# Kernel optimization log

Hardware: AMD Instinct MI355X
Metric: run time of the kernel (lower is better)

The kernel has to match this reference:

```python
import jax, jax.numpy as jnp
import numpy as np

N_NODES = 100000
HIDDEN = 64
IN_CH = 128
N_EDGES = 1600000


def setup_inputs() -> dict:
    key = jax.random.key(0)
    ks = jax.random.split(key, 12)
    x = jax.random.normal(ks[0], (N_NODES, IN_CH), dtype=jnp.float32)
    edge_index = jax.random.randint(ks[1], (2, N_EDGES), 0, N_NODES, dtype=jnp.int64)

    def glorot(k, fan_in, fan_out):
        s = jnp.sqrt(6.0 / (fan_in + fan_out)).astype(jnp.float32)
        return jax.random.uniform(k, (fan_in, fan_out), jnp.float32, -s, s)

    return {
        "x": x,
        "edge_index": edge_index,
        # GCNConv layer 1: linear (no bias) + post-aggregation bias
        "W1": glorot(ks[2], IN_CH, HIDDEN),
        "b1": jnp.zeros((HIDDEN,), jnp.float32),
        # GCNConv layer 2
        "W2": glorot(ks[3], HIDDEN, HIDDEN),
        "b2": jnp.zeros((HIDDEN,), jnp.float32),
        # edge classifier MLP: Linear(2H,H) -> ReLU -> Linear(H,2)
        "Wc1": glorot(ks[4], 2 * HIDDEN, HIDDEN),
        "bc1": jnp.zeros((HIDDEN,), jnp.float32),
        "Wc2": glorot(ks[5], HIDDEN, 2),
        "bc2": jnp.zeros((2,), jnp.float32),
    }


def _gcn_forward(x, edge_index, W1, b1, W2, b2, Wc1, bc1, Wc2, bc2):
    n = x.shape[0]
    src, dst = edge_index[0], edge_index[1]
    # add self-loops (PyG GCNConv default)
    loop = jnp.arange(n, dtype=edge_index.dtype)
    a_src = jnp.concatenate([src, loop])  # [E+N]
    a_dst = jnp.concatenate([dst, loop])
    # symmetric normalization: deg over destination with unit edge weights
    deg = jax.ops.segment_sum(jnp.ones(a_dst.shape[0], x.dtype), a_dst, num_segments=n)
    dis = jax.lax.rsqrt(deg)  # deg >= 1 due to self-loops
    norm = dis[a_src] * dis[a_dst]  # [E+N]

    def conv(h, W, b):
        h = h @ W  # [N, H]
        msg = h[a_src] * norm[:, None]  # [E+N, H] gather + scale
        return jax.ops.segment_sum(msg, a_dst, num_segments=n) + b

    h = jax.nn.relu(conv(x, W1, b1))  # dropout is identity in eval mode
    h = conv(h, W2, b2)
    # edge classifier on concatenated endpoint embeddings
    e = jnp.concatenate([h[src], h[dst]], axis=1)  # [E, 2H]
    z = jax.nn.relu(e @ Wc1 + bc1)
    return z @ Wc2 + bc2  # [E, 2]


def reference(x, edge_index, W1, b1, W2, b2, Wc1, bc1, Wc2, bc2):
    return _gcn_forward(x, edge_index, W1, b1, W2, b2, Wc1, bc1, Wc2, bc2)
```

## Files before the change

### kernel.cpp

```cpp
#include <hip/hip_runtime.h>
#include <hip/hip_fp16.h>

#define HID 64
#define BKT_SHIFT 10
#define BKT_NODES 1024
#define PCHUNKS 512

typedef _Float16 half8 __attribute__((ext_vector_type(8)));
typedef _Float16 half4 __attribute__((ext_vector_type(4)));
typedef float f32x4 __attribute__((ext_vector_type(4)));
typedef float f32x2 __attribute__((ext_vector_type(2)));

__global__ __launch_bounds__(256) void k_bkt_count(const int* __restrict__ dst,
                                                   int* __restrict__ G, int E,
                                                   int nbkt, int chunk) {
  __shared__ int hist[128];
  int p = blockIdx.x, tid = threadIdx.x;
  for (int i = tid; i < nbkt; i += 256) hist[i] = 0;
  __syncthreads();
  int s = p * chunk, e = min(s + chunk, E);
  for (int i = s + tid; i < e; i += 256) atomicAdd(&hist[dst[i] >> BKT_SHIFT], 1);
  __syncthreads();
  for (int b = tid; b < nbkt; b += 256) G[b * PCHUNKS + p] = hist[b];
}

__global__ void k_scan1(const int* __restrict__ in, int* __restrict__ scanout,
                        int* __restrict__ blocksums, int n) {
  __shared__ int sdata[256];
  int tid = threadIdx.x;
  int base = blockIdx.x * 1024 + tid * 4;
  int v0 = 0, v1 = 0, v2 = 0, v3 = 0;
  if (base + 0 < n) v0 = in[base + 0];
  if (base + 1 < n) v1 = in[base + 1];
  if (base + 2 < n) v2 = in[base + 2];
  if (base + 3 < n) v3 = in[base + 3];
  int tsum = v0 + v1 + v2 + v3;
  sdata[tid] = tsum;
  __syncthreads();
  for (int off = 1; off < 256; off <<= 1) {
    int t = (tid >= off) ? sdata[tid - off] : 0;
    __syncthreads();
    sdata[tid] += t;
    __syncthreads();
  }
  int excl = sdata[tid] - tsum;
  if (base + 0 < n) scanout[base + 0] = excl;
  if (base + 1 < n) scanout[base + 1] = excl + v0;
  if (base + 2 < n) scanout[base + 2] = excl + v0 + v1;
  if (base + 3 < n) scanout[base + 3] = excl + v0 + v1 + v2;
  if (tid == 255) blocksums[blockIdx.x] = sdata[255];
}

__global__ void k_scan2(int* blocksums, int nb) {
  __shared__ int s[128];
  int tid = threadIdx.x;
  int v = (tid < nb) ? blocksums[tid] : 0;
  s[tid] = v;
  __syncthreads();
  for (int off = 1; off < 128; off <<= 1) {
    int t = (tid >= off) ? s[tid - off] : 0;
    __syncthreads();
    s[tid] += t;
    __syncthreads();
  }
  if (tid < nb) blocksums[tid] = s[tid] - v;
}

__global__ void k_scan3(const int* __restrict__ scanout,
                        const int* __restrict__ blocksums, int* __restrict__ outp,
                        int n) {
  int i = blockIdx.x * blockDim.x + threadIdx.x;
  if (i < n) outp[i] = scanout[i] + blocksums[i >> 10];
}

__global__ __launch_bounds__(256) void k_bkt_scatter(
    const int* __restrict__ src, const int* __restrict__ dst,
    const int* __restrict__ Gscan, int* __restrict__ psrc,
    unsigned short* __restrict__ pdst, int E, int nbkt, int chunk) {
  __shared__ int gbase[128];
  __shared__ int rcnt[128];
  int p = blockIdx.x, tid = threadIdx.x;
  for (int b = tid; b < nbkt; b += 256) {
    gbase[b] = Gscan[b * PCHUNKS + p];
    rcnt[b] = 0;
  }
  __syncthreads();
  int s = p * chunk, e = min(s + chunk, E);
  for (int i = s + tid; i < e; i += 256) {
    int d = dst[i];
    int b = d >> BKT_SHIFT;
    int r = atomicAdd(&rcnt[b], 1);
    int pos = gbase[b] + r;
    psrc[pos] = src[i];
    pdst[pos] = (unsigned short)(d & (BKT_NODES - 1));
  }
}

__global__ __launch_bounds__(1024) void k_bkt_final(
    const int* __restrict__ Gscan, const int* __restrict__ psrc,
    const unsigned short* __restrict__ pdst, int* __restrict__ rowoff,
    float* __restrict__ dis, int* __restrict__ csr_src, int E, int nbkt, int N) {
  __shared__ int cnt[BKT_NODES];
  __shared__ int lo[BKT_NODES];
  int b = blockIdx.x, tid = threadIdx.x;
  int s = Gscan[b * PCHUNKS];
  int eend = (b + 1 < nbkt) ? Gscan[(b + 1) * PCHUNKS] : E;
  cnt[tid] = 0;
  __syncthreads();
  for (int i = s + tid; i < eend; i += 1024) atomicAdd(&cnt[pdst[i]], 1);
  __syncthreads();
  int v = cnt[tid];
  lo[tid] = v;
  __syncthreads();
  for (int off = 1; off < 1024; off <<= 1) {
    int t = (tid >= off) ? lo[tid - off] : 0;
    __syncthreads();
    lo[tid] += t;
    __syncthreads();
  }
  int excl = lo[tid] - v;
  int node = b * BKT_NODES + tid;
  if (node < N) {
    rowoff[node] = s + excl;
    dis[node] = rsqrtf((float)v + 1.0f);
  }
  __syncthreads();
  lo[tid] = excl;
  cnt[tid] = 0;
  __syncthreads();
  for (int i = s + tid; i < eend; i += 1024) {
    int ln = pdst[i];
    int r = atomicAdd(&cnt[ln], 1);
    csr_src[s + lo[ln] + r] = psrc[i];
  }
}

__global__ void k_pack_all(const float* __restrict__ W1, const float* __restrict__ W2,
                           const float* __restrict__ Wc1, const float* __restrict__ bc1,
                           __half* __restrict__ packW1, __half* __restrict__ packW2,
                           __half* __restrict__ packUV, float* __restrict__ biasUV,
                           __half* __restrict__ ysent) {
  int b = blockIdx.x, tid = threadIdx.x;
  if (b < 4) {
    int t = b * 256 + tid;
    int f = t >> 6, L = t & 63;
    int kc = f >> 2, nb = f & 3;
    int k = 32 * kc + ((L >> 4) << 3);
    int n = (L & 15) + 16 * nb;
    for (int j = 0; j < 8; ++j)
      packW1[(t << 3) + j] = __float2half(W1[(k + j) * 64 + n]);
  } else if (b < 6) {
    int t = (b - 4) * 256 + tid;
    int f = t >> 6, L = t & 63;
    int kc = f >> 2, nb = f & 3;
    int k = 32 * kc + ((L >> 4) << 3);
    int n = (L & 15) + 16 * nb;
    for (int j = 0; j < 8; ++j)
      packW2[(t << 3) + j] = __float2half(W2[(k + j) * 64 + n]);
  } else if (b < 10) {
    int t = (b - 6) * 256 + tid;
    int f = t >> 6, L = t & 63;
    int kc = f >> 3, nb = f & 7;
    int k = 32 * kc + ((L >> 4) << 3);
    int n = (L & 15) + 16 * nb;
    for (int j = 0; j < 8; ++j) {
      float w = (n < 64) ? Wc1[(k + j) * 64 + n] : Wc1[(64 + k + j) * 64 + (n - 64)];
      packUV[(t << 3) + j] = __float2half(w);
    }
  } else {
    if (tid < 128) biasUV[tid] = (tid < 64) ? bc1[tid] : 0.f;
    else if (tid < 192) ysent[tid - 128] = __float2half(0.f);
  }
}

template <int K, int NOUT, bool F32IN>
__global__ __launch_bounds__(256) void k_lin_mfma(
    const void* __restrict__ Xv, const __half* __restrict__ packB,
    const float* __restrict__ bias, const float* __restrict__ dis,
    __half* __restrict__ Y, int n) {
  int wid = blockIdx.x * 4 + (threadIdx.x >> 6);
  int rowbase = wid * 16;
  if (rowbase >= n) return;
  int L = threadIdx.x & 63;
  int m16 = L & 15, quad = L >> 4;
  constexpr int KC = K / 32;
  constexpr int NB = NOUT / 16;

  half8 Bf[KC * NB];
  const half8* packv = (const half8*)packB;
#pragma unroll
  for (int f = 0; f < KC * NB; ++f) Bf[f] = packv[f * 64 + L];

  int r = min(rowbase + m16, n - 1);
  half8 Af[KC];
  if (F32IN) {
    const float* xr = (const float*)Xv + (long)r * K;
#pragma unroll
    for (int kc = 0; kc < KC; ++kc) {
      const float4* xp = (const float4*)(xr + kc * 32 + quad * 8);
      float4 a = xp[0], b = xp[1];
      half8 v = {(_Float16)a.x, (_Float16)a.y, (_Float16)a.z, (_Float16)a.w,
                 (_Float16)b.x, (_Float16)b.y, (_Float16)b.z, (_Float16)b.w};
      Af[kc] = v;
    }
  } else {
    const half8* xr = (const half8*)((const __half*)Xv + (long)r * K);
#pragma unroll
    for (int kc = 0; kc < KC; ++kc) Af[kc] = xr[kc * 4 + quad];
  }

  f32x4 acc[NB];
#pragma unroll
  for (int nb = 0; nb < NB; ++nb) acc[nb] = {0.f, 0.f, 0.f, 0.f};
#pragma unroll
  for (int kc = 0; kc < KC; ++kc)
#pragma unroll
    for (int nb = 0; nb < NB; ++nb)
      acc[nb] = __builtin_amdgcn_mfma_f32_16x16x32_f16(Af[kc], Bf[kc * NB + nb],
                                                       acc[nb], 0, 0, 0);

  float dv[4];
#pragma unroll
  for (int j = 0; j < 4; ++j) {
    int ro = rowbase + quad * 4 + j;
    dv[j] = (dis && ro < n) ? dis[ro] : 1.f;
  }
#pragma unroll
  for (int nb = 0; nb < NB; ++nb) {
    int col = m16 + 16 * nb;
    float bv = bias ? bias[col] : 0.f;
#pragma unroll
    for (int j = 0; j < 4; ++j) {
      int ro = rowbase + quad * 4 + j;
      if (ro < n) {
        float v = (acc[nb][j] + bv) * dv[j];
        Y[(long)ro * NOUT + col] = __float2half(v);
      }
    }
  }
}

__global__ __launch_bounds__(256) void k_agg_csr(
    const __half* __restrict__ Yh, const float* __restrict__ dis,
    const int* __restrict__ rowoff, const int* __restrict__ csr_src,
    const float* __restrict__ b, __half* __restrict__ A, int n, int E, int relu) {
  int node = blockIdx.x * 4 + (threadIdx.x >> 6);
  if (node >= n) return;
  int L = threadIdx.x & 63;
  int sub = L >> 4;
  int cq = L & 15;
  const half4* Y4 = (const half4*)Yh;
  float dd = dis[node];
  int i0 = rowoff[node];
  int end = (node == n - 1) ? E : rowoff[node + 1];

  float z[4][4] = {{0.f}};
  if (sub == 0) {
    half4 hv = Y4[(long)node * 16 + cq];
#pragma unroll
    for (int j = 0; j < 4; ++j) z[0][j] = (float)hv[j];
  }

  int last = end - 1;
  for (int base = i0; base < end; base += 16) {
    int sidx[4];
#pragma unroll
    for (int slot = 0; slot < 4; ++slot) {
      int idx = base + slot * 4 + sub;
      int sl = csr_src[min(idx, last)];
      sidx[slot] = (idx < end) ? sl : n;
    }
#pragma unroll
    for (int slot = 0; slot < 4; ++slot) {
      half4 hv = Y4[(long)sidx[slot] * 16 + cq];
#pragma unroll
      for (int j = 0; j < 4; ++j) z[slot][j] += (float)hv[j];
    }
  }

  float a[4];
#pragma unroll
  for (int j = 0; j < 4; ++j) {
    a[j] = (z[0][j] + z[1][j]) + (z[2][j] + z[3][j]);
    a[j] += __shfl_xor(a[j], 16, 64);
    a[j] += __shfl_xor(a[j], 32, 64);
  }
  if (sub == 0) {
    float4 bb = ((const float4*)b)[cq];
    float v0 = fmaf(a[0], dd, bb.x), v1 = fmaf(a[1], dd, bb.y);
    float v2 = fmaf(a[2], dd, bb.z), v3 = fmaf(a[3], dd, bb.w);
    if (relu) {
      v0 = fmaxf(v0, 0.f); v1 = fmaxf(v1, 0.f);
      v2 = fmaxf(v2, 0.f); v3 = fmaxf(v3, 0.f);
    }
    half4 o = {(_Float16)v0, (_Float16)v1, (_Float16)v2, (_Float16)v3};
    ((half4*)A)[(long)node * 16 + cq] = o;
  }
}

__global__ __launch_bounds__(256) void k_edge_mlp(
    const __half* __restrict__ UV, const int* __restrict__ src,
    const int* __restrict__ dst, const float* __restrict__ Wc2,
    const float* __restrict__ bc2, float* __restrict__ out, int E, int nwaves) {
  int wid = blockIdx.x * 4 + (threadIdx.x >> 6);
  int L = threadIdx.x & 63;
  int g = L >> 3;
  int cg = L & 7;

  float w0[8], w1[8];
#pragma unroll
  for (int j = 0; j < 8; ++j) {
    int c = cg * 8 + j;
    w0[j] = Wc2[2 * c];
    w1[j] = Wc2[2 * c + 1];
  }
  float ob0 = bc2[0], ob1 = bc2[1];

  const half8* UV8 = (const half8*)UV;
  int last = E - 1;
  const half8 hzero = {(_Float16)0, (_Float16)0, (_Float16)0, (_Float16)0,
                       (_Float16)0, (_Float16)0, (_Float16)0, (_Float16)0};

  for (long base = (long)wid * 32; base < E; base += (long)nwaves * 32) {
    int se[4], de[4];
#pragma unroll
    for (int s = 0; s < 4; ++s) {
      int e = (int)base + s * 8 + g;
      int ec = min(e, last);
      se[s] = __builtin_nontemporal_load(&src[ec]);
      de[s] = __builtin_nontemporal_load(&dst[ec]);
    }
    half8 uu[4], vv[4];
#pragma unroll
    for (int s = 0; s < 4; ++s) {
      uu[s] = UV8[(long)se[s] * 16 + cg];
      vv[s] = UV8[(long)de[s] * 16 + 8 + cg];
    }
#pragma unroll
    for (int s = 0; s < 4; ++s) {
      half8 t = uu[s] + vv[s];
      t = __builtin_elementwise_max(t, hzero);
      float o0 = 0.f, o1 = 0.f;
#pragma unroll
      for (int j = 0; j < 8; ++j) {
        float tv = (float)t[j];
        o0 = fmaf(tv, w0[j], o0);
        o1 = fmaf(tv, w1[j], o1);
      }
      o0 += __shfl_xor(o0, 1, 64);
      o1 += __shfl_xor(o1, 1, 64);
      o0 += __shfl_xor(o0, 2, 64);
      o1 += __shfl_xor(o1, 2, 64);
      o0 += __shfl_xor(o0, 4, 64);
      o1 += __shfl_xor(o1, 4, 64);
      int e = (int)base + s * 8 + g;
      if (cg == 0 && e < E) {
        f32x2 o = {o0 + ob0, o1 + ob1};
        __builtin_nontemporal_store(o, (f32x2*)(out + 2 * (long)e));
      }
    }
  }
}

extern "C" void kernel_launch(void* const* d_in, const int* in_sizes, int n_in,
                              void* d_out, int out_size, void* d_ws, size_t ws_size,
                              hipStream_t stream) {
  const float* x   = (const float*)d_in[0];
  const int*   ei  = (const int*)d_in[1];
  const float* W1  = (const float*)d_in[2];
  const float* b1  = (const float*)d_in[3];
  const float* W2  = (const float*)d_in[4];
  const float* b2  = (const float*)d_in[5];
  const float* Wc1 = (const float*)d_in[6];
  const float* bc1 = (const float*)d_in[7];
  const float* Wc2 = (const float*)d_in[8];
  const float* bc2 = (const float*)d_in[9];

  const int N = in_sizes[0] / 128;
  const int E = in_sizes[1] / 2;
  const int* src = ei;
  const int* dst = ei + E;

  const int nbkt = (N + BKT_NODES - 1) >> BKT_SHIFT;
  const int gsz = nbkt * PCHUNKS;
  const int chunk = (E + PCHUNKS - 1) / PCHUNKS;

  float* dis     = (float*)d_ws;
  __half* y      = (__half*)(dis + N);
  __half* h      = y + (long)(N + 1) * HID;
  __half* UV     = h + (long)N * HID;
  __half* packW1 = UV + (long)N * 128;
  __half* packW2 = packW1 + 8192;
  __half* packUV = packW2 + 4096;
  float* biasUV  = (float*)(packUV + 8192);
  int* rowoff    = (int*)(biasUV + 128);
  int* csr_src   = rowoff + N;
  int* G         = csr_src + E;
  int* Gs1       = G + gsz;
  int* Gbs       = Gs1 + gsz;
  int* Gscan     = Gbs + 128;
  int* psrc            = (int*)UV;
  unsigned short* pdst = (unsigned short*)(psrc + E);

  const int B = 256;
  int nbScan = (gsz + 1023) / 1024;

  k_pack_all<<<11, B, 0, stream>>>(W1, W2, Wc1, bc1, packW1, packW2, packUV,
                                   biasUV, y + (long)N * HID);
  k_bkt_count<<<PCHUNKS, B, 0, stream>>>(dst, G, E, nbkt, chunk);
  k_scan1<<<nbScan, B, 0, stream>>>(G, Gs1, Gbs, gsz);
  k_scan2<<<1, 128, 0, stream>>>(Gbs, nbScan);
  k_scan3<<<(gsz + B - 1) / B, B, 0, stream>>>(Gs1, Gbs, Gscan, gsz);
  k_bkt_scatter<<<PCHUNKS, B, 0, stream>>>(src, dst, Gscan, psrc, pdst, E, nbkt,
                                           chunk);
  k_bkt_final<<<nbkt, 1024, 0, stream>>>(Gscan, psrc, pdst, rowoff, dis, csr_src,
                                         E, nbkt, N);

  int gAgg = (N + 3) / 4;
  int gLin = (N + 63) / 64;

  k_lin_mfma<128, 64, true><<<gLin, B, 0, stream>>>(x, packW1, nullptr, dis, y, N);
  k_agg_csr<<<gAgg, B, 0, stream>>>(y, dis, rowoff, csr_src, b1, h, N, E, 1);

  k_lin_mfma<64, 64, false><<<gLin, B, 0, stream>>>(h, packW2, nullptr, dis, y, N);
  k_agg_csr<<<gAgg, B, 0, stream>>>(y, dis, rowoff, csr_src, b2, h, N, E, 0);

  k_lin_mfma<64, 128, false><<<gLin, B, 0, stream>>>(h, packUV, biasUV, nullptr, UV, N);
  int cblocks = 2048;
  int nwaves = cblocks * 4;
  k_edge_mlp<<<cblocks, B, 0, stream>>>(UV, src, dst, Wc2, bc2,
                                        (float*)d_out, E, nwaves);
}
```

Baseline: 354.6 us.

## Run edge MLP per destination node over CSR with permuted edge ids

The edge classifier now walks the destination-sorted CSR, one wave per node. Each wave loads the node's V half once and gathers only the source-side U rows. To write results in original edge order, the bucket sort now also carries each edge's original index (peid/csr_eid), and outputs are stored scattered by that index. This removes the per-edge dst gather, at the cost of extra sort traffic, uncoalesced 8-byte output stores, and load imbalance from uneven node degrees.

```diff
diff --git a/kernel.cpp b/kernel.cpp
--- a/kernel.cpp
+++ b/kernel.cpp
@@ -76,7 +76,8 @@
 __global__ __launch_bounds__(256) void k_bkt_scatter(
     const int* __restrict__ src, const int* __restrict__ dst,
     const int* __restrict__ Gscan, int* __restrict__ psrc,
-    unsigned short* __restrict__ pdst, int E, int nbkt, int chunk) {
+    unsigned short* __restrict__ pdst, int* __restrict__ peid, int E, int nbkt,
+    int chunk) {
   __shared__ int gbase[128];
   __shared__ int rcnt[128];
   int p = blockIdx.x, tid = threadIdx.x;
@@ -93,13 +94,15 @@
     int pos = gbase[b] + r;
     psrc[pos] = src[i];
     pdst[pos] = (unsigned short)(d & (BKT_NODES - 1));
+    peid[pos] = i;
   }
 }
 
 __global__ __launch_bounds__(1024) void k_bkt_final(
     const int* __restrict__ Gscan, const int* __restrict__ psrc,
-    const unsigned short* __restrict__ pdst, int* __restrict__ rowoff,
-    float* __restrict__ dis, int* __restrict__ csr_src, int E, int nbkt, int N) {
+    const unsigned short* __restrict__ pdst, const int* __restrict__ peid,
+    int* __restrict__ rowoff, float* __restrict__ dis, int* __restrict__ csr_src,
+    int* __restrict__ csr_eid, int E, int nbkt, int N) {
   __shared__ int cnt[BKT_NODES];
   __shared__ int lo[BKT_NODES];
   int b = blockIdx.x, tid = threadIdx.x;
@@ -131,7 +134,9 @@
   for (int i = s + tid; i < eend; i += 1024) {
     int ln = pdst[i];
     int r = atomicAdd(&cnt[ln], 1);
-    csr_src[s + lo[ln] + r] = psrc[i];
+    int pos = s + lo[ln] + r;
+    csr_src[pos] = psrc[i];
+    csr_eid[pos] = peid[i];
   }
 }
 
@@ -298,11 +303,13 @@
   }
 }
 
-__global__ __launch_bounds__(256) void k_edge_mlp(
-    const __half* __restrict__ UV, const int* __restrict__ src,
-    const int* __restrict__ dst, const float* __restrict__ Wc2,
-    const float* __restrict__ bc2, float* __restrict__ out, int E, int nwaves) {
-  int wid = blockIdx.x * 4 + (threadIdx.x >> 6);
+__global__ __launch_bounds__(256) void k_edge_mlp_csr(
+    const __half* __restrict__ UV, const int* __restrict__ rowoff,
+    const int* __restrict__ csr_src, const int* __restrict__ csr_eid,
+    const float* __restrict__ Wc2, const float* __restrict__ bc2,
+    float* __restrict__ out, int n, int E) {
+  int node = blockIdx.x * 4 + (threadIdx.x >> 6);
+  if (node >= n) return;
   int L = threadIdx.x & 63;
   int g = L >> 3;
   int cg = L & 7;
@@ -317,47 +324,38 @@
   float ob0 = bc2[0], ob1 = bc2[1];
 
   const half8* UV8 = (const half8*)UV;
-  int last = E - 1;
+  half8 vv = UV8[(long)node * 16 + 8 + cg];
   const half8 hzero = {(_Float16)0, (_Float16)0, (_Float16)0, (_Float16)0,
                        (_Float16)0, (_Float16)0, (_Float16)0, (_Float16)0};
 
-  for (long base = (long)wid * 32; base < E; base += (long)nwaves * 32) {
-    int se[4], de[4];
-#pragma unroll
-    for (int s = 0; s < 4; ++s) {
-      int e = (int)base + s * 8 + g;
-      int ec = min(e, last);
-      se[s] = __builtin_nontemporal_load(&src[ec]);
-      de[s] = __builtin_nontemporal_load(&dst[ec]);
-    }
-    half8 uu[4], vv[4];
-#pragma unroll
-    for (int s = 0; s < 4; ++s) {
-      uu[s] = UV8[(long)se[s] * 16 + cg];
-      vv[s] = UV8[(long)de[s] * 16 + 8 + cg];
-    }
-#pragma unroll
-    for (int s = 0; s < 4; ++s) {
-      half8 t = uu[s] + vv[s];
-      t = __builtin_elementwise_max(t, hzero);
-      float o0 = 0.f, o1 = 0.f;
-#pragma unroll
-      for (int j = 0; j < 8; ++j) {
-        float tv = (float)t[j];
-        o0 = fmaf(tv, w0[j], o0);
-        o1 = fmaf(tv, w1[j], o1);
-      }
-      o0 += __shfl_xor(o0, 1, 64);
-      o1 += __shfl_xor(o1, 1, 64);
-      o0 += __shfl_xor(o0, 2, 64);
-      o1 += __shfl_xor(o1, 2, 64);
-      o0 += __shfl_xor(o0, 4, 64);
-      o1 += __shfl_xor(o1, 4, 64);
-      int e = (int)base + s * 8 + g;
-      if (cg == 0 && e < E) {
-        f32x2 o = {o0 + ob0, o1 + ob1};
-        __builtin_nontemporal_store(o, (f32x2*)(out + 2 * (long)e));
-      }
+  int i0 = rowoff[node];
+  int end = (node == n - 1) ? E : rowoff[node + 1];
+  int last = end - 1;
+
+  for (int base = i0; base < end; base += 8) {
+    int idx = base + g;
+    int ec = min(idx, last);
+    int s = __builtin_nontemporal_load(&csr_src[ec]);
+    int eid = __builtin_nontemporal_load(&csr_eid[ec]);
+    half8 uu = UV8[(long)s * 16 + cg];
+    half8 t = uu + vv;
+    t = __builtin_elementwise_max(t, hzero);
+    float o0 = 0.f, o1 = 0.f;
+#pragma unroll
+    for (int j = 0; j < 8; ++j) {
+      float tv = (float)t[j];
+      o0 = fmaf(tv, w0[j], o0);
+      o1 = fmaf(tv, w1[j], o1);
+    }
+    o0 += __shfl_xor(o0, 1, 64);
+    o1 += __shfl_xor(o1, 1, 64);
+    o0 += __shfl_xor(o0, 2, 64);
+    o1 += __shfl_xor(o1, 2, 64);
+    o0 += __shfl_xor(o0, 4, 64);
+    o1 += __shfl_xor(o1, 4, 64);
+    if (cg == 0 && idx < end) {
+      f32x2 o = {o0 + ob0, o1 + ob1};
+      __builtin_nontemporal_store(o, (f32x2*)(out + 2 * (long)eid));
     }
   }
 }
@@ -399,8 +397,10 @@
   int* Gs1       = G + gsz;
   int* Gbs       = Gs1 + gsz;
   int* Gscan     = Gbs + 128;
+  int* csr_eid   = Gscan + gsz;
   int* psrc            = (int*)UV;
   unsigned short* pdst = (unsigned short*)(psrc + E);
+  int* peid            = (int*)(pdst + E);
 
   const int B = 256;
   int nbScan = (gsz + 1023) / 1024;
@@ -411,10 +411,10 @@
   k_scan1<<<nbScan, B, 0, stream>>>(G, Gs1, Gbs, gsz);
   k_scan2<<<1, 128, 0, stream>>>(Gbs, nbScan);
   k_scan3<<<(gsz + B - 1) / B, B, 0, stream>>>(Gs1, Gbs, Gscan, gsz);
-  k_bkt_scatter<<<PCHUNKS, B, 0, stream>>>(src, dst, Gscan, psrc, pdst, E, nbkt,
-                                           chunk);
-  k_bkt_final<<<nbkt, 1024, 0, stream>>>(Gscan, psrc, pdst, rowoff, dis, csr_src,
-                                         E, nbkt, N);
+  k_bkt_scatter<<<PCHUNKS, B, 0, stream>>>(src, dst, Gscan, psrc, pdst, peid, E,
+                                           nbkt, chunk);
+  k_bkt_final<<<nbkt, 1024, 0, stream>>>(Gscan, psrc, pdst, peid, rowoff, dis,
+                                         csr_src, csr_eid, E, nbkt, N);
 
   int gAgg = (N + 3) / 4;
   int gLin = (N + 63) / 64;
@@ -426,8 +426,6 @@
   k_agg_csr<<<gAgg, B, 0, stream>>>(y, dis, rowoff, csr_src, b2, h, N, E, 0);
 
   k_lin_mfma<64, 128, false><<<gLin, B, 0, stream>>>(h, packUV, biasUV, nullptr, UV, N);
-  int cblocks = 2048;
-  int nwaves = cblocks * 4;
-  k_edge_mlp<<<cblocks, B, 0, stream>>>(UV, src, dst, Wc2, bc2,
-                                        (float*)d_out, E, nwaves);
-}
+  k_edge_mlp_csr<<<gAgg, B, 0, stream>>>(UV, rowoff, csr_src, csr_eid, Wc2, bc2,
+                                         (float*)d_out, N, E);
+}
```

Result: slower. 399.3 us (+12.6%).
